# Kernel tuning notes

Hardware: AMD Instinct MI355X
Metric: run time of the kernel (lower is better)

## Reference

```python
import jax, jax.numpy as jnp
import numpy as np

D_MODEL = 256
D_INNER = 512   # expand * d_model
NHEADS = 8
HEADDIM = 64    # d_inner // nheads
NGROUPS = 1
MDIST = 16


def setup_inputs() -> dict:
    key = jax.random.key(0)
    ks = jax.random.split(key, 12)
    B, L, Q = 4, 2048, 300
    in_key = jax.random.normal(ks[0], (B, L, D_MODEL), jnp.float32)
    in_query = jax.random.normal(ks[1], (B, Q, D_MODEL), jnp.float32)
    dist = jax.random.normal(ks[2], (B, L, Q, MDIST), jnp.float32)

    def lin(k, out_f, in_f):  # torch nn.Linear default init (kaiming-uniform-ish)
        bound = 1.0 / np.sqrt(in_f)
        return jax.random.uniform(k, (out_f, in_f), jnp.float32, -bound, bound)

    W_key = lin(ks[3], 2 * D_INNER + 2 * NGROUPS + NHEADS, D_MODEL)
    W_query = lin(ks[4], D_INNER, D_MODEL)
    W_bc = lin(ks[5], 2 * NGROUPS, MDIST)
    W_dt = lin(ks[6], NHEADS, MDIST)
    # dt_bias init (inverse-softplus of dt sampled log-uniform in [1e-4, 0.1])
    dt_min, dt_max = 1e-4, 0.1
    dtv = jnp.exp(jax.random.uniform(ks[7], (NHEADS,)) * (np.log(dt_max) - np.log(dt_min)) + np.log(dt_min))
    dtv = jnp.clip(dtv, 1e-4, None)
    dt_bias = dtv + jnp.log(-jnp.expm1(-dtv))
    A_log = jnp.log(jax.random.uniform(ks[8], (NHEADS,), minval=1.0, maxval=16.0))
    Dp = jnp.ones((NHEADS,), jnp.float32)
    W_out_key = lin(ks[9], D_MODEL, D_INNER)
    W_out_query = lin(ks[10], D_MODEL, D_INNER)
    key_norm_w = jnp.ones((D_INNER,), jnp.float32)
    ln_w = jnp.ones((D_INNER,), jnp.float32)
    ln_b = jnp.zeros((D_INNER,), jnp.float32)
    return dict(in_key=in_key, in_query=in_query, dist=dist, W_key=W_key, W_query=W_query,
                W_bc=W_bc, W_dt=W_dt, dt_bias=dt_bias, A_log=A_log, Dp=Dp,
                W_out_key=W_out_key, W_out_query=W_out_query, key_norm_w=key_norm_w,
                ln_w=ln_w, ln_b=ln_b)


def _issm_scan(x, S0, dt, A, Bm, Cm, Dp):
    """Selective scan with per-(l,h,n) dt and per-(l,n) B,C (ngroups=1).
    x: (B,L,H,P)  dt: (B,L,H,N)  Bm,Cm: (B,L,N)  S0: (B,H,P,N)  A: (H,)  Dp: (H,)
    """
    xs = (jnp.moveaxis(x, 1, 0), jnp.moveaxis(dt, 1, 0),
          jnp.moveaxis(Bm, 1, 0), jnp.moveaxis(Cm, 1, 0))

    def step(S, inp):
        xl, dtl, Bl, Cl = inp               # (B,H,P), (B,H,N), (B,N), (B,N)
        dA = jnp.exp(dtl * A[None, :, None])            # (B,H,N)
        dBx = (dtl * Bl[:, None, :])[:, :, None, :] * xl[:, :, :, None]
        S = S * dA[:, :, None, :] + dBx                 # (B,H,P,N)
        y = jnp.einsum('bhpn,bn->bhp', S, Cl) + Dp[None, :, None] * xl
        return S, y

    Sf, ys = jax.lax.scan(step, S0, xs)
    return jnp.moveaxis(ys, 0, 1), Sf       # (B,L,H,P), (B,H,P,N)


def reference(in_key, in_query, dist, W_key, W_query, W_bc, W_dt, dt_bias, A_log, Dp,
              W_out_key, W_out_query, key_norm_w, ln_w, ln_b):
    B, L, _ = in_key.shape
    Q = in_query.shape[1]
    zxbcdt = in_key @ W_key.T                            # (B,L,2*Din+2g+H)
    z = zxbcdt[..., :D_INNER]
    x = zxbcdt[..., D_INNER:2 * D_INNER].reshape(B, L, NHEADS, HEADDIM)
    b_bias = zxbcdt[..., 2 * D_INNER:2 * D_INNER + 1]    # (B,L,1)
    c_bias = zxbcdt[..., 2 * D_INNER + 1:2 * D_INNER + 2]
    dt_proj_bias = zxbcdt[..., 2 * D_INNER + 2:]         # (B,L,H)

    # initial state: (B,H,P,Q) -- state dim N == num_queries
    S0 = (in_query @ W_query.T).reshape(B, Q, NHEADS, HEADDIM).transpose(0, 2, 3, 1)
    A = -jnp.exp(A_log)                                  # (H,), constant over state dim

    bc = jnp.einsum('blqm,cm->blqc', dist, W_bc)         # (B,L,Q,2)
    Bm = bc[..., 0] + b_bias                             # (B,L,Q)
    Cm = bc[..., 1] + c_bias
    dtb = jnp.einsum('blqm,hm->blhq', dist, W_dt)        # (B,L,H,Q)
    dt = jax.nn.softplus(dtb + dt_proj_bias[..., None] + dt_bias[None, None, :, None])

    y_f, S_f = _issm_scan(x, S0, dt, A, Bm, Cm, Dp)
    # bidirectional: backward branch uses identical (cloned) x/B/C, flipped along L
    y_b, S_b = _issm_scan(x[:, ::-1], S0, dt[:, ::-1], A, Bm[:, ::-1], Cm[:, ::-1], Dp)
    y = (y_f + y_b[:, ::-1]) * 0.5
    S = (S_f + S_b) * 0.5

    key = y.reshape(B, L, D_INNER)
    g = key * jax.nn.silu(z)                             # gated RMSNorm, norm_before_gate=False
    key = g * jax.lax.rsqrt(jnp.mean(g * g, -1, keepdims=True) + 1e-5) * key_norm_w
    out_key = key @ W_out_key.T

    ls = S.transpose(0, 3, 1, 2).reshape(B, Q, D_INNER)  # b h p q -> b q (h p)
    mu = jnp.mean(ls, -1, keepdims=True)
    var = jnp.mean((ls - mu) ** 2, -1, keepdims=True)
    ls = (ls - mu) * jax.lax.rsqrt(var + 1e-5) * ln_w + ln_b
    out_query = ls @ W_out_query.T
    return out_key, out_query
```

## Files before the change

kernel.cpp:

```cpp
#include <hip/hip_runtime.h>
#include <hip/hip_bf16.h>

#define D_MODEL 256
#define D_INNER 512
#define NHEADS 8
#define HEADDIM 64
#define MDIST 16
#define BB 4
#define LL 2048
#define QQ 300
#define QP 320
#define NSEG 16
#define SEGLEN 128

typedef unsigned short ushort_t;
typedef __attribute__((ext_vector_type(8))) short bf16x8;
typedef __attribute__((ext_vector_type(4))) float f32x4;

__device__ __forceinline__ void bf16_split(float v, ushort_t& hi, ushort_t& lo) {
    __hip_bfloat16 h = __float2bfloat16(v);
    float hf = __bfloat162float(h);
    __hip_bfloat16 l = __float2bfloat16(v - hf);
    hi = *(ushort_t*)&h;
    lo = *(ushort_t*)&l;
}
__device__ __forceinline__ ushort_t us_of_bf16(float v) {
    __hip_bfloat16 h = __float2bfloat16(v);
    return *(ushort_t*)&h;
}
__device__ __forceinline__ float bflo(unsigned u) { return __uint_as_float(u << 16); }
__device__ __forceinline__ float bfhi(unsigned u) { return __uint_as_float(u & 0xffff0000u); }

__global__ __launch_bounds__(256) void c_split(const float* __restrict__ in,
                                               ushort_t* __restrict__ hi,
                                               ushort_t* __restrict__ lo, int n) {
    int i = blockIdx.x * 256 + threadIdx.x;
    if (i >= n) return;
    ushort_t h, l;
    bf16_split(in[i], h, l);
    hi[i] = h;
    lo[i] = l;
}

__global__ __launch_bounds__(256) void gemm_bf16s(const ushort_t* __restrict__ Ah,
                                                  const ushort_t* __restrict__ Al,
                                                  const ushort_t* __restrict__ Bh,
                                                  const ushort_t* __restrict__ Bl,
                                                  float* __restrict__ C,
                                                  int M, int N, int K) {
    int w = threadIdx.x >> 6, lane = threadIdx.x & 63;
    int n0 = blockIdx.x * 64;
    int m0 = blockIdx.y * 128 + w * 32;
    int lm = lane & 15, lk = (lane >> 4) * 8;
    f32x4 acc[2][4];
#pragma unroll
    for (int i = 0; i < 2; i++)
#pragma unroll
        for (int j = 0; j < 4; j++) acc[i][j] = {0.f, 0.f, 0.f, 0.f};

    for (int k0 = 0; k0 < K; k0 += 32) {
        bf16x8 ah[2], al[2], bh[4], blo[4];
#pragma unroll
        for (int mf = 0; mf < 2; mf++) {
            int row = m0 + mf * 16 + lm;
            if (row >= M) row = M - 1;
            size_t off = (size_t)row * K + k0 + lk;
            ah[mf] = *(const bf16x8*)(Ah + off);
            al[mf] = *(const bf16x8*)(Al + off);
        }
#pragma unroll
        for (int nf = 0; nf < 4; nf++) {
            int col = n0 + nf * 16 + lm;
            size_t off = (size_t)col * K + k0 + lk;
            bh[nf]  = *(const bf16x8*)(Bh + off);
            blo[nf] = *(const bf16x8*)(Bl + off);
        }
#pragma unroll
        for (int mf = 0; mf < 2; mf++)
#pragma unroll
            for (int nf = 0; nf < 4; nf++) {
                acc[mf][nf] = __builtin_amdgcn_mfma_f32_16x16x32_bf16(ah[mf], bh[nf],  acc[mf][nf], 0, 0, 0);
                acc[mf][nf] = __builtin_amdgcn_mfma_f32_16x16x32_bf16(ah[mf], blo[nf], acc[mf][nf], 0, 0, 0);
                acc[mf][nf] = __builtin_amdgcn_mfma_f32_16x16x32_bf16(al[mf], bh[nf],  acc[mf][nf], 0, 0, 0);
            }
    }
#pragma unroll
    for (int mf = 0; mf < 2; mf++)
#pragma unroll
        for (int nf = 0; nf < 4; nf++)
#pragma unroll
            for (int r = 0; r < 4; r++) {
                int m = m0 + mf * 16 + (lane >> 4) * 4 + r;
                if (m < M) C[(size_t)m * N + n0 + nf * 16 + lm] = acc[mf][nf][r];
            }
}

__global__ __launch_bounds__(256) void k1b_bias(const float* __restrict__ in_key,
                                                const float* __restrict__ W_key,
                                                float* __restrict__ bias10) {
    int w = threadIdx.x >> 6, lane = threadIdx.x & 63;
    int row = blockIdx.x * 4 + w;
    float4 a = *(const float4*)(in_key + (size_t)row * 256 + lane * 4);
#pragma unroll
    for (int c = 0; c < 10; c++) {
        float4 b = *(const float4*)(W_key + (size_t)(1024 + c) * 256 + lane * 4);
        float t = a.x * b.x + a.y * b.y + a.z * b.z + a.w * b.w;
#pragma unroll
        for (int o = 32; o > 0; o >>= 1) t += __shfl_down(t, o, 64);
        if (lane == 0) bias10[row * 10 + c] = t;
    }
}

__global__ __launch_bounds__(256) void k2_dist(const float* __restrict__ dist,
                                               const float* __restrict__ bias10,
                                               const float* __restrict__ W_bc,
                                               const float* __restrict__ W_dt,
                                               const float* __restrict__ dt_bias,
                                               const float* __restrict__ A_log,
                                               float* __restrict__ dA,
                                               ushort_t* __restrict__ dtBh,
                                               ushort_t* __restrict__ Cmh) {
    __shared__ float sWbc[32], sWdt[128], sb[8], sA[8];
    int tid = threadIdx.x;
    if (tid < 32) sWbc[tid] = W_bc[tid];
    else if (tid < 160) sWdt[tid - 32] = W_dt[tid - 32];
    else if (tid < 168) sb[tid - 160] = dt_bias[tid - 160];
    else if (tid < 176) sA[tid - 168] = -expf(A_log[tid - 168]);
    __syncthreads();
    int gid = blockIdx.x * 256 + tid;
    if (gid >= BB * LL * QQ) return;
    int q = gid % QQ;
    int bl = gid / QQ;
    const float* dp = dist + (size_t)gid * 16;
    float d[16];
    float4 d0 = *(const float4*)(dp + 0);
    float4 d1 = *(const float4*)(dp + 4);
    float4 d2 = *(const float4*)(dp + 8);
    float4 d3 = *(const float4*)(dp + 12);
    d[0]=d0.x; d[1]=d0.y; d[2]=d0.z; d[3]=d0.w;
    d[4]=d1.x; d[5]=d1.y; d[6]=d1.z; d[7]=d1.w;
    d[8]=d2.x; d[9]=d2.y; d[10]=d2.z; d[11]=d2.w;
    d[12]=d3.x; d[13]=d3.y; d[14]=d3.z; d[15]=d3.w;
    float bc0 = 0.f, bc1 = 0.f;
#pragma unroll
    for (int m = 0; m < 16; m++) {
        bc0 = fmaf(d[m], sWbc[m], bc0);
        bc1 = fmaf(d[m], sWbc[16 + m], bc1);
    }
    float Bmv = bc0 + bias10[bl * 10 + 0];
    float Cv  = bc1 + bias10[bl * 10 + 1];
    Cmh[bl * QP + q] = us_of_bf16(Cv);
#pragma unroll
    for (int h = 0; h < 8; h++) {
        float t = 0.f;
#pragma unroll
        for (int m = 0; m < 16; m++) t = fmaf(d[m], sWdt[h * 16 + m], t);
        float pre = t + bias10[bl * 10 + 2 + h] + sb[h];
        float dt = (pre > 20.f) ? pre : log1pf(expf(pre));
        int o = (bl * 8 + h) * QP + q;
        dA[o]   = expf(sA[h] * dt);
        dtBh[o] = us_of_bf16(dt * Bmv);
    }
}

__global__ __launch_bounds__(256) void k2b_segdecay(const float* __restrict__ dA,
                                                    float* __restrict__ segd) {
    int gid = blockIdx.x * 256 + threadIdx.x;
    if (gid >= BB * NSEG * 8 * QP) return;
    int q = gid % QP; int r = gid / QP;
    int h = r % 8; r /= 8;
    int s = r % NSEG; int b = r / NSEG;
    int base = ((b * LL + s * SEGLEN) * 8 + h) * QP + q;
    float p = 1.f;
    for (int i = 0; i < SEGLEN; i++) p *= dA[base + i * 8 * QP];
    segd[gid] = p;
}

__global__ __launch_bounds__(512) void pass_ac(const float* __restrict__ dA,
                                               const ushort_t* __restrict__ dtBh,
                                               const ushort_t* __restrict__ Cmh,
                                               const float* __restrict__ zx,
                                               float* __restrict__ S_local,
                                               float* __restrict__ yf,
                                               float* __restrict__ yb) {
    __shared__ __align__(16) unsigned char sOp[2][2][2816];
    __shared__ float ybuf[2][2][8][64];
    int seg = blockIdx.x, bh = blockIdx.y, dir = blockIdx.z;
    int tid = threadIdx.x;
    int w = tid >> 6, lane = tid & 63;
    int n0 = w * 40;
    int b = bh >> 3, h = bh & 7;
    float S[40];
#pragma unroll
    for (int j = 0; j < 40; j++) S[j] = 0.f;
    float* __restrict__ yo = dir ? yb : yf;

    auto stage = [&](int g, int buf) {
        if (tid < 352) {
            int it = (tid >= 176) ? 1 : 0;
            int q = tid - 176 * it;
            int i = g * 2 + it;
            int l = dir ? (LL - 1 - (seg * SEGLEN + i)) : (seg * SEGLEN + i);
            int bl = b * LL + l;
            const uint4* src;
            if (q < 80)       src = (const uint4*)(dA   + (size_t)(bl * 8 + h) * QP) + q;
            else if (q < 120) src = (const uint4*)(dtBh + (size_t)(bl * 8 + h) * QP) + (q - 80);
            else if (q < 160) src = (const uint4*)(Cmh  + (size_t)bl * QP) + (q - 120);
            else              src = (const uint4*)(zx + (size_t)bl * 1024 + 512 + h * 64) + (q - 160);
            ((uint4*)sOp[buf][it])[q] = *src;
        }
    };
    stage(0, 0);
    const int NG = SEGLEN / 2;
    for (int g = 0; g < NG; g++) {
        __syncthreads();
        if (g + 1 < NG) stage(g + 1, (g + 1) & 1);
        if (g > 0 && tid < 128) {
            int it = tid >> 6, p = tid & 63;
            int i = (g - 1) * 2 + it;
            int l = dir ? (LL - 1 - (seg * SEGLEN + i)) : (seg * SEGLEN + i);
            int bl = b * LL + l;
            const float* yb0 = &ybuf[(g - 1) & 1][it][0][p];
            float t = 0.f;
#pragma unroll
            for (int ww = 0; ww < 8; ww++) t += yb0[ww * 64];
            yo[(size_t)(bl * 8 + h) * 64 + p] = t;
        }
#pragma unroll
        for (int it = 0; it < 2; it++) {
            const unsigned char* bufc = sOp[g & 1][it];
            const float* pA = (const float*)bufc + n0;
            const ushort_t* pB = (const ushort_t*)(bufc + 1280) + n0;
            const ushort_t* pC = (const ushort_t*)(bufc + 1920) + n0;
            float x = ((const float*)(bufc + 2560))[lane];
            float y = 0.f;
#pragma unroll
            for (int c = 0; c < 5; c++) {
                float4 a0 = *(const float4*)(pA + c * 8);
                float4 a1 = *(const float4*)(pA + c * 8 + 4);
                uint4 bw = *(const uint4*)(pB + c * 8);
                uint4 cw = *(const uint4*)(pC + c * 8);
                int j = c * 8;
                S[j+0] = fmaf(S[j+0], a0.x, bflo(bw.x) * x); y = fmaf(S[j+0], bflo(cw.x), y);
                S[j+1] = fmaf(S[j+1], a0.y, bfhi(bw.x) * x); y = fmaf(S[j+1], bfhi(cw.x), y);
                S[j+2] = fmaf(S[j+2], a0.z, bflo(bw.y) * x); y = fmaf(S[j+2], bflo(cw.y), y);
                S[j+3] = fmaf(S[j+3], a0.w, bfhi(bw.y) * x); y = fmaf(S[j+3], bfhi(cw.y), y);
                S[j+4] = fmaf(S[j+4], a1.x, bflo(bw.z) * x); y = fmaf(S[j+4], bflo(cw.z), y);
                S[j+5] = fmaf(S[j+5], a1.y, bfhi(bw.z) * x); y = fmaf(S[j+5], bfhi(cw.z), y);
                S[j+6] = fmaf(S[j+6], a1.z, bflo(bw.w) * x); y = fmaf(S[j+6], bflo(cw.w), y);
                S[j+7] = fmaf(S[j+7], a1.w, bfhi(bw.w) * x); y = fmaf(S[j+7], bfhi(cw.w), y);
            }
            ybuf[g & 1][it][w][lane] = y;
        }
    }
    __syncthreads();
    if (tid < 128) {
        int it = tid >> 6, p = tid & 63;
        int i = (NG - 1) * 2 + it;
        int l = dir ? (LL - 1 - (seg * SEGLEN + i)) : (seg * SEGLEN + i);
        int bl = b * LL + l;
        const float* yb0 = &ybuf[1][it][0][p];
        float t = 0.f;
#pragma unroll
        for (int ww = 0; ww < 8; ww++) t += yb0[ww * 64];
        yo[(size_t)(bl * 8 + h) * 64 + p] = t;
    }
    size_t base = (size_t)((dir * NSEG + seg) * 32 + bh) * QP * 64;
#pragma unroll
    for (int j = 0; j < 40; j++)
        S_local[base + (size_t)(n0 + j) * 64 + lane] = S[j];
}

__global__ __launch_bounds__(256) void pass_b(const float* __restrict__ S_local,
                                              const float* __restrict__ segd,
                                              const float* __restrict__ S0q,
                                              float* __restrict__ S_in,
                                              float* __restrict__ Savg) {
    int gid = blockIdx.x * 256 + threadIdx.x;
    if (gid >= BB * 8 * QP * 64) return;
    int p = gid & 63; int r = gid >> 6;
    int n = r % QP; r /= QP;
    int h = r & 7; int b = r >> 3;
    int bh = b * 8 + h;
    float s0 = (n < QQ) ? S0q[(size_t)(b * QQ + n) * 512 + h * 64 + p] : 0.f;
    float Sf = 0.f, Sb = 0.f;
    for (int dir = 0; dir < 2; dir++) {
        float S = s0;
        for (int s = 0; s < NSEG; s++) {
            size_t idx = (size_t)(((dir * NSEG + s) * 32 + bh) * QP + n) * 64 + p;
            S_in[idx] = S;
            int sf = dir ? (NSEG - 1 - s) : s;
            float dec = segd[((b * NSEG + sf) * 8 + h) * QP + n];
            S = fmaf(S, dec, S_local[idx]);
        }
        if (dir == 0) Sf = S; else Sb = S;
    }
    Savg[((bh) * QP + n) * 64 + p] = 0.5f * (Sf + Sb);
}

__global__ __launch_bounds__(256) void k3_corr(const float* __restrict__ dA,
                                               const ushort_t* __restrict__ Cmh,
                                               const float* __restrict__ Sin,
                                               float* __restrict__ yf,
                                               float* __restrict__ yb) {
    __shared__ __align__(16) ushort_t sAh[128][48], sAl[128][48];
    __shared__ __align__(16) ushort_t sBh[64][48], sBl[64][48];
    __shared__ float pref[8][32];
    int seg = blockIdx.x, bh = blockIdx.y, dir = blockIdx.z;
    int b = bh >> 3, h = bh & 7;
    int tid = threadIdx.x;
    int w = tid >> 6, lane = tid & 63;
    int lm = lane & 15, lkq = lane >> 4;
    f32x4 acc[2][4];
#pragma unroll
    for (int i = 0; i < 2; i++)
#pragma unroll
        for (int j = 0; j < 4; j++) acc[i][j] = {0.f, 0.f, 0.f, 0.f};
    size_t sinBase = (size_t)((dir * NSEG + seg) * 32 + bh) * QP * 64;
    int nl = tid & 31, iseg = tid >> 5;

    for (int k0 = 0; k0 < QP; k0 += 32) {
        __syncthreads();
#pragma unroll
        for (int r = 0; r < 8; r++) {
            int flat = tid + r * 256;
            int kn = flat >> 6, p = flat & 63;
            float v = Sin[sinBase + (size_t)(k0 + kn) * 64 + p];
            ushort_t hi, lo;
            bf16_split(v, hi, lo);
            sBh[p][kn] = hi;
            sBl[p][kn] = lo;
        }
        float da[16], cm[16];
#pragma unroll
        for (int k = 0; k < 16; k++) {
            int i = iseg * 16 + k;
            int l = dir ? (LL - 1 - (seg * SEGLEN + i)) : (seg * SEGLEN + i);
            int bl = b * LL + l;
            da[k] = dA[(size_t)(bl * 8 + h) * QP + k0 + nl];
            cm[k] = __uint_as_float((unsigned)Cmh[(size_t)bl * QP + k0 + nl] << 16);
        }
        float lp = 1.f;
#pragma unroll
        for (int k = 0; k < 16; k++) lp *= da[k];
        pref[iseg][nl] = lp;
        __syncthreads();
        if (tid < 32) {
            float c = 1.f;
#pragma unroll
            for (int s = 0; s < 8; s++) {
                float t = pref[s][tid];
                pref[s][tid] = c;
                c *= t;
            }
        }
        __syncthreads();
        float cum = pref[iseg][nl];
#pragma unroll
        for (int k = 0; k < 16; k++) {
            cum *= da[k];
            float v = cum * cm[k];
            ushort_t hi, lo;
            bf16_split(v, hi, lo);
            int i = iseg * 16 + k;
            sAh[i][nl] = hi;
            sAl[i][nl] = lo;
        }
        __syncthreads();
        bf16x8 ah[2], al[2], bhf[4], blf[4];
#pragma unroll
        for (int mf = 0; mf < 2; mf++) {
            int row = w * 32 + mf * 16 + lm;
            ah[mf] = *(const bf16x8*)&sAh[row][lkq * 8];
            al[mf] = *(const bf16x8*)&sAl[row][lkq * 8];
        }
#pragma unroll
        for (int nf = 0; nf < 4; nf++) {
            int p = nf * 16 + lm;
            bhf[nf] = *(const bf16x8*)&sBh[p][lkq * 8];
            blf[nf] = *(const bf16x8*)&sBl[p][lkq * 8];
        }
#pragma unroll
        for (int mf = 0; mf < 2; mf++)
#pragma unroll
            for (int nf = 0; nf < 4; nf++) {
                acc[mf][nf] = __builtin_amdgcn_mfma_f32_16x16x32_bf16(ah[mf], bhf[nf], acc[mf][nf], 0, 0, 0);
                acc[mf][nf] = __builtin_amdgcn_mfma_f32_16x16x32_bf16(ah[mf], blf[nf], acc[mf][nf], 0, 0, 0);
                acc[mf][nf] = __builtin_amdgcn_mfma_f32_16x16x32_bf16(al[mf], bhf[nf], acc[mf][nf], 0, 0, 0);
            }
    }
    float* __restrict__ yo = dir ? yb : yf;
#pragma unroll
    for (int mf = 0; mf < 2; mf++)
#pragma unroll
        for (int nf = 0; nf < 4; nf++)
#pragma unroll
            for (int r = 0; r < 4; r++) {
                int i = w * 32 + mf * 16 + lkq * 4 + r;
                int p = nf * 16 + lm;
                int l = dir ? (LL - 1 - (seg * SEGLEN + i)) : (seg * SEGLEN + i);
                size_t idx = (size_t)((b * LL + l) * 8 + h) * 64 + p;
                yo[idx] += acc[mf][nf][r];
            }
}

__global__ __launch_bounds__(512) void k4_gate(const float* __restrict__ yf,
                                               const float* __restrict__ yb,
                                               const float* __restrict__ zx,
                                               const float* __restrict__ Dp,
                                               const float* __restrict__ knw,
                                               ushort_t* __restrict__ kh,
                                               ushort_t* __restrict__ kl) {
    int bl = blockIdx.x;
    int t = threadIdx.x;
    int h = t >> 6;
    float x = zx[(size_t)bl * 1024 + 512 + t];
    float yv = 0.5f * (yf[(size_t)bl * 512 + t] + yb[(size_t)bl * 512 + t]) + Dp[h] * x;
    float z = zx[(size_t)bl * 1024 + t];
    float g = yv * (z / (1.f + expf(-z)));
    float v = g * g;
#pragma unroll
    for (int o = 32; o > 0; o >>= 1) v += __shfl_down(v, o, 64);
    __shared__ float rs[8];
    __shared__ float stot;
    if ((t & 63) == 0) rs[t >> 6] = v;
    __syncthreads();
    if (t == 0) {
        float s = 0.f;
#pragma unroll
        for (int i = 0; i < 8; i++) s += rs[i];
        stot = s;
    }
    __syncthreads();
    float rms = rsqrtf(stot / 512.f + 1e-5f);
    float kv = g * rms * knw[t];
    ushort_t hi, lo;
    bf16_split(kv, hi, lo);
    kh[(size_t)bl * 512 + t] = hi;
    kl[(size_t)bl * 512 + t] = lo;
}

__global__ __launch_bounds__(512) void k5_ln(const float* __restrict__ Savg,
                                             const float* __restrict__ lnw,
                                             const float* __restrict__ lnb,
                                             ushort_t* __restrict__ lh,
                                             ushort_t* __restrict__ ll) {
    int bq = blockIdx.x;
    int b = bq / QQ, q = bq % QQ;
    int t = threadIdx.x;
    int h = t >> 6, p = t & 63;
    float v = Savg[((b * 8 + h) * QP + q) * 64 + p];
    float s1 = v, s2 = v * v;
#pragma unroll
    for (int o = 32; o > 0; o >>= 1) {
        s1 += __shfl_down(s1, o, 64);
        s2 += __shfl_down(s2, o, 64);
    }
    __shared__ float r1[8], r2[8];
    __shared__ float smu, srv;
    if ((t & 63) == 0) { r1[t >> 6] = s1; r2[t >> 6] = s2; }
    __syncthreads();
    if (t == 0) {
        float a = 0.f, c = 0.f;
#pragma unroll
        for (int i = 0; i < 8; i++) { a += r1[i]; c += r2[i]; }
        float mu = a / 512.f;
        float var = c / 512.f - mu * mu;
        smu = mu;
        srv = rsqrtf(var + 1e-5f);
    }
    __syncthreads();
    float ov = (v - smu) * srv * lnw[t] + lnb[t];
    ushort_t hi, lo;
    bf16_split(ov, hi, lo);
    lh[(size_t)bq * 512 + t] = hi;
    ll[(size_t)bq * 512 + t] = lo;
}

extern "C" void kernel_launch(void* const* d_in, const int* in_sizes, int n_in,
                              void* d_out, int out_size, void* d_ws, size_t ws_size,
                              hipStream_t stream) {
    const float* in_key    = (const float*)d_in[0];
    const float* in_query  = (const float*)d_in[1];
    const float* dist      = (const float*)d_in[2];
    const float* W_key     = (const float*)d_in[3];
    const float* W_query   = (const float*)d_in[4];
    const float* W_bc      = (const float*)d_in[5];
    const float* W_dt      = (const float*)d_in[6];
    const float* dt_bias   = (const float*)d_in[7];
    const float* A_log     = (const float*)d_in[8];
    const float* Dp        = (const float*)d_in[9];
    const float* W_out_key = (const float*)d_in[10];
    const float* W_out_query = (const float*)d_in[11];
    const float* key_norm_w = (const float*)d_in[12];
    const float* ln_w      = (const float*)d_in[13];
    const float* ln_b      = (const float*)d_in[14];

    float* out_key = (float*)d_out;
    float* out_query = out_key + (size_t)BB * LL * D_MODEL;

    char* w8 = (char*)d_ws;
    auto alloc = [&](size_t bytes) {
        char* ptr = w8;
        w8 += (bytes + 255) & ~(size_t)255;
        return ptr;
    };
    float* zx     = (float*)alloc((size_t)8192 * 1024 * 4);
    float* bias10 = (float*)alloc((size_t)8192 * 10 * 4);
    float* S0q    = (float*)alloc((size_t)1200 * 512 * 4);
    float* dAb    = (float*)alloc((size_t)8192 * 8 * QP * 4);
    ushort_t* dtBb = (ushort_t*)alloc((size_t)8192 * 8 * QP * 2);
    ushort_t* Cmb  = (ushort_t*)alloc((size_t)8192 * QP * 2);
    float* segd   = (float*)alloc((size_t)BB * NSEG * 8 * QP * 4);
    float* Sloc   = (float*)alloc((size_t)2 * NSEG * 32 * QP * 64 * 4);
    float* Sin    = (float*)alloc((size_t)2 * NSEG * 32 * QP * 64 * 4);
    float* yfb    = (float*)alloc((size_t)8192 * 512 * 4);
    float* ybb    = (float*)alloc((size_t)8192 * 512 * 4);
    float* Savg   = (float*)alloc((size_t)32 * QP * 64 * 4);
    ushort_t* ink_h  = (ushort_t*)alloc((size_t)2097152 * 2);
    ushort_t* ink_l  = (ushort_t*)alloc((size_t)2097152 * 2);
    ushort_t* wk_h   = (ushort_t*)alloc((size_t)262144 * 2);
    ushort_t* wk_l   = (ushort_t*)alloc((size_t)262144 * 2);
    ushort_t* inq_h  = (ushort_t*)alloc((size_t)307200 * 2);
    ushort_t* inq_l  = (ushort_t*)alloc((size_t)307200 * 2);
    ushort_t* wq_h   = (ushort_t*)alloc((size_t)131072 * 2);
    ushort_t* wq_l   = (ushort_t*)alloc((size_t)131072 * 2);
    ushort_t* keyb_h = (ushort_t*)alloc((size_t)4194304 * 2);
    ushort_t* keyb_l = (ushort_t*)alloc((size_t)4194304 * 2);
    ushort_t* wok_h  = (ushort_t*)alloc((size_t)131072 * 2);
    ushort_t* wok_l  = (ushort_t*)alloc((size_t)131072 * 2);
    ushort_t* lsn_h  = (ushort_t*)alloc((size_t)614400 * 2);
    ushort_t* lsn_l  = (ushort_t*)alloc((size_t)614400 * 2);
    ushort_t* woq_h  = (ushort_t*)alloc((size_t)131072 * 2);
    ushort_t* woq_l  = (ushort_t*)alloc((size_t)131072 * 2);

    c_split<<<8192, 256, 0, stream>>>(in_key, ink_h, ink_l, 2097152);
    c_split<<<1024, 256, 0, stream>>>(W_key, wk_h, wk_l, 262144);
    c_split<<<1200, 256, 0, stream>>>(in_query, inq_h, inq_l, 307200);
    c_split<<<512, 256, 0, stream>>>(W_query, wq_h, wq_l, 131072);
    c_split<<<512, 256, 0, stream>>>(W_out_key, wok_h, wok_l, 131072);
    c_split<<<512, 256, 0, stream>>>(W_out_query, woq_h, woq_l, 131072);

    gemm_bf16s<<<dim3(16, 64), 256, 0, stream>>>(ink_h, ink_l, wk_h, wk_l, zx, 8192, 1024, 256);
    k1b_bias<<<2048, 256, 0, stream>>>(in_key, W_key, bias10);
    gemm_bf16s<<<dim3(8, 10), 256, 0, stream>>>(inq_h, inq_l, wq_h, wq_l, S0q, 1200, 512, 256);

    k2_dist<<<9600, 256, 0, stream>>>(dist, bias10, W_bc, W_dt, dt_bias, A_log, dAb, dtBb, Cmb);
    k2b_segdecay<<<640, 256, 0, stream>>>(dAb, segd);

    pass_ac<<<dim3(NSEG, 32, 2), 512, 0, stream>>>(dAb, dtBb, Cmb, zx, Sloc, yfb, ybb);
    pass_b<<<2560, 256, 0, stream>>>(Sloc, segd, S0q, Sin, Savg);
    k3_corr<<<dim3(NSEG, 32, 2), 256, 0, stream>>>(dAb, Cmb, Sin, yfb, ybb);

    k4_gate<<<8192, 512, 0, stream>>>(yfb, ybb, zx, Dp, key_norm_w, keyb_h, keyb_l);
    gemm_bf16s<<<dim3(4, 64), 256, 0, stream>>>(keyb_h, keyb_l, wok_h, wok_l, out_key, 8192, 256, 512);

    k5_ln<<<1200, 512, 0, stream>>>(Savg, ln_w, ln_b, lsn_h, lsn_l);
    gemm_bf16s<<<dim3(4, 10), 256, 0, stream>>>(lsn_h, lsn_l, woq_h, woq_l, out_query, 1200, 256, 512);
}
```

Baseline: 1.061 ms.

## Read scan operands directly via wave-uniform scalar loads instead of LDS staging

The chunked scan pass no longer stages dA, dtB, C and x through double-buffered shared memory. Each wave now loads its 40-state slice straight from global memory, with the wave index made uniform via readfirstlane so the operand loads can become scalar loads. Synchronisation drops from one barrier per two timesteps to one per eight, and the y reduction is spread across all eight waves. The trade-off is that global-load latency is no longer hidden by the explicit prefetch and now sits on the recurrence's critical path.

```diff
diff --git a/kernel.cpp b/kernel.cpp
--- a/kernel.cpp
+++ b/kernel.cpp
@@ -183,11 +183,11 @@
                                                float* __restrict__ S_local,
                                                float* __restrict__ yf,
                                                float* __restrict__ yb) {
-    __shared__ __align__(16) unsigned char sOp[2][2][2816];
-    __shared__ float ybuf[2][2][8][64];
+    __shared__ float ybuf[2][8][8][64];
     int seg = blockIdx.x, bh = blockIdx.y, dir = blockIdx.z;
     int tid = threadIdx.x;
-    int w = tid >> 6, lane = tid & 63;
+    int w = __builtin_amdgcn_readfirstlane(tid >> 6);
+    int lane = tid & 63;
     int n0 = w * 40;
     int b = bh >> 3, h = bh & 7;
     float S[40];
@@ -195,75 +195,41 @@
     for (int j = 0; j < 40; j++) S[j] = 0.f;
     float* __restrict__ yo = dir ? yb : yf;
 
-    auto stage = [&](int g, int buf) {
-        if (tid < 352) {
-            int it = (tid >= 176) ? 1 : 0;
-            int q = tid - 176 * it;
-            int i = g * 2 + it;
+    for (int blk = 0; blk < 16; blk++) {
+        for (int it = 0; it < 8; it++) {
+            int i = blk * 8 + it;
             int l = dir ? (LL - 1 - (seg * SEGLEN + i)) : (seg * SEGLEN + i);
             int bl = b * LL + l;
-            const uint4* src;
-            if (q < 80)       src = (const uint4*)(dA   + (size_t)(bl * 8 + h) * QP) + q;
-            else if (q < 120) src = (const uint4*)(dtBh + (size_t)(bl * 8 + h) * QP) + (q - 80);
-            else if (q < 160) src = (const uint4*)(Cmh  + (size_t)bl * QP) + (q - 120);
-            else              src = (const uint4*)(zx + (size_t)bl * 1024 + 512 + h * 64) + (q - 160);
-            ((uint4*)sOp[buf][it])[q] = *src;
-        }
-    };
-    stage(0, 0);
-    const int NG = SEGLEN / 2;
-    for (int g = 0; g < NG; g++) {
+            int ob = (bl * 8 + h) * QP + n0;
+            const float* __restrict__ pa = dA + ob;
+            const unsigned* __restrict__ pb = (const unsigned*)(dtBh + ob);
+            const unsigned* __restrict__ pc = (const unsigned*)(Cmh + bl * QP + n0);
+            float x = zx[(size_t)bl * 1024 + 512 + h * 64 + lane];
+            float y = 0.f;
+#pragma unroll
+            for (int c = 0; c < 20; c++) {
+                float a0 = pa[2 * c], a1 = pa[2 * c + 1];
+                unsigned ub = pb[c], uc = pc[c];
+                float t0 = bflo(ub) * x;
+                float t1 = bfhi(ub) * x;
+                S[2 * c]     = fmaf(S[2 * c],     a0, t0);
+                y = fmaf(S[2 * c],     bflo(uc), y);
+                S[2 * c + 1] = fmaf(S[2 * c + 1], a1, t1);
+                y = fmaf(S[2 * c + 1], bfhi(uc), y);
+            }
+            ybuf[blk & 1][it][w][lane] = y;
+        }
         __syncthreads();
-        if (g + 1 < NG) stage(g + 1, (g + 1) & 1);
-        if (g > 0 && tid < 128) {
-            int it = tid >> 6, p = tid & 63;
-            int i = (g - 1) * 2 + it;
+        {
+            int i = blk * 8 + w;
             int l = dir ? (LL - 1 - (seg * SEGLEN + i)) : (seg * SEGLEN + i);
             int bl = b * LL + l;
-            const float* yb0 = &ybuf[(g - 1) & 1][it][0][p];
+            const float* yb0 = &ybuf[blk & 1][w][0][lane];
             float t = 0.f;
 #pragma unroll
             for (int ww = 0; ww < 8; ww++) t += yb0[ww * 64];
-            yo[(size_t)(bl * 8 + h) * 64 + p] = t;
-        }
-#pragma unroll
-        for (int it = 0; it < 2; it++) {
-            const unsigned char* bufc = sOp[g & 1][it];
-            const float* pA = (const float*)bufc + n0;
-            const ushort_t* pB = (const ushort_t*)(bufc + 1280) + n0;
-            const ushort_t* pC = (const ushort_t*)(bufc + 1920) + n0;
-            float x = ((const float*)(bufc + 2560))[lane];
-            float y = 0.f;
-#pragma unroll
-            for (int c = 0; c < 5; c++) {
-                float4 a0 = *(const float4*)(pA + c * 8);
-                float4 a1 = *(const float4*)(pA + c * 8 + 4);
-                uint4 bw = *(const uint4*)(pB + c * 8);
-                uint4 cw = *(const uint4*)(pC + c * 8);
-                int j = c * 8;
-                S[j+0] = fmaf(S[j+0], a0.x, bflo(bw.x) * x); y = fmaf(S[j+0], bflo(cw.x), y);
-                S[j+1] = fmaf(S[j+1], a0.y, bfhi(bw.x) * x); y = fmaf(S[j+1], bfhi(cw.x), y);
-                S[j+2] = fmaf(S[j+2], a0.z, bflo(bw.y) * x); y = fmaf(S[j+2], bflo(cw.y), y);
-                S[j+3] = fmaf(S[j+3], a0.w, bfhi(bw.y) * x); y = fmaf(S[j+3], bfhi(cw.y), y);
-                S[j+4] = fmaf(S[j+4], a1.x, bflo(bw.z) * x); y = fmaf(S[j+4], bflo(cw.z), y);
-                S[j+5] = fmaf(S[j+5], a1.y, bfhi(bw.z) * x); y = fmaf(S[j+5], bfhi(cw.z), y);
-                S[j+6] = fmaf(S[j+6], a1.z, bflo(bw.w) * x); y = fmaf(S[j+6], bflo(cw.w), y);
-                S[j+7] = fmaf(S[j+7], a1.w, bfhi(bw.w) * x); y = fmaf(S[j+7], bfhi(cw.w), y);
-            }
-            ybuf[g & 1][it][w][lane] = y;
-        }
-    }
-    __syncthreads();
-    if (tid < 128) {
-        int it = tid >> 6, p = tid & 63;
-        int i = (NG - 1) * 2 + it;
-        int l = dir ? (LL - 1 - (seg * SEGLEN + i)) : (seg * SEGLEN + i);
-        int bl = b * LL + l;
-        const float* yb0 = &ybuf[1][it][0][p];
-        float t = 0.f;
-#pragma unroll
-        for (int ww = 0; ww < 8; ww++) t += yb0[ww * 64];
-        yo[(size_t)(bl * 8 + h) * 64 + p] = t;
+            yo[(size_t)(bl * 8 + h) * 64 + lane] = t;
+        }
     }
     size_t base = (size_t)((dir * NSEG + seg) * 32 + bh) * QP * 64;
 #pragma unroll
```

New measurement: 964.1 us. 1.1x faster.
